# Optimization experiments

Hardware: AMD Instinct MI355X
Metric: run time of the kernel (lower is better)

The kernel has to match this reference:

```python
import jax, jax.numpy as jnp
import numpy as np

B, S, F = 32, 4096, 256
G, N = 2, 128           # num_groups, num_entries_per_group
D = F // G              # group_dim = 128
E = 256                 # embed_dim


def setup_inputs() -> dict:
    key = jax.random.key(0)
    ks = jax.random.split(key, 6)
    return {
        "features": jax.random.normal(ks[0], (B, S, F), jnp.float32),
        "gumbel": jax.random.gumbel(ks[1], (B, S, G, N), jnp.float32),
        "W_logits": jax.random.normal(ks[2], (G, D, N), jnp.float32) * (1.0 / np.sqrt(D)),
        "b_logits": jnp.zeros((G, N), jnp.float32),
        "codebooks": jax.random.normal(ks[3], (G, N, D), jnp.float32) * 0.02,
        "W_out": jax.random.normal(ks[4], (F, E), jnp.float32) * (1.0 / np.sqrt(F)),
        "b_out": jnp.zeros((E,), jnp.float32),
    }


def reference(features, gumbel, W_logits, b_logits, codebooks, W_out, b_out):
    b, s, f = features.shape
    grouped = features.reshape(b, s, G, D)                       # [B,S,G,D]
    logits = jnp.einsum("bsgd,gdn->bsgn", grouped, W_logits) + b_logits
    noisy = logits + gumbel                                      # training=True
    soft = jax.nn.softmax(noisy, axis=-1)                        # [B,S,G,N]
    hard_idx = jnp.argmax(noisy, axis=-1)                        # [B,S,G] int
    hard = jax.nn.one_hot(hard_idx, N, dtype=soft.dtype)
    st = jax.lax.stop_gradient(hard - soft) + soft               # straight-through
    quantized = jnp.einsum("bsgn,gnd->bsgd", st, codebooks)      # [B,S,G,D]
    quantized = quantized.reshape(b, s, G * D)                   # [B,S,F]
    out = quantized @ W_out + b_out                              # [B,S,E]
    indices = hard_idx.astype(jnp.int32)                         # [B,S,G]
    return out, indices
```

## Files before the change

kernel.cpp:

```cpp
#include <hip/hip_runtime.h>

#define T_TOTAL (32 * 4096)
#define FDIM 256
#define NG 2
#define NN 128
#define DDIM 128
#define EDIM 256

#define TAU 0.004f
#define CAP 16384

typedef __attribute__((ext_vector_type(4))) float f32x4;
typedef __attribute__((ext_vector_type(8))) short short8;

__global__ __launch_bounds__(256) void prep_kernel(
    const float* __restrict__ codebooks,
    const float* __restrict__ W_out,
    const float* __restrict__ Wl,
    float* __restrict__ CO,
    short* __restrict__ BT,
    int* __restrict__ flag_count)
{
    const int gn  = blockIdx.x;
    const int g   = gn >> 7;
    const int tid = threadIdx.x;
    __shared__ float cb[DDIM];
    if (tid < DDIM) cb[tid] = codebooks[gn * DDIM + tid];
    if (tid >= 128) {
        const int k = tid - 128;
        const int n = gn & 127;
        const float x = Wl[((size_t)g * DDIM + k) * NN + n];
        const unsigned u = __float_as_uint(x);
        const float hi = __uint_as_float(u & 0xffff0000u);
        const unsigned u2 = __float_as_uint(x - hi);
        BT[(size_t)g * 16384 + n * 128 + k] = (short)(u >> 16);
        BT[32768 + (size_t)g * 16384 + n * 128 + k] = (short)(u2 >> 16);
    }
    if (gn == 0 && tid == 0) *flag_count = 0;
    __syncthreads();
    float acc = 0.f;
    const float* wcol = W_out + (g * DDIM) * EDIM + tid;
#pragma unroll 4
    for (int d = 0; d < DDIM; ++d) acc += cb[d] * wcol[d * EDIM];
    CO[gn * EDIM + tid] = acc;
}

__global__ __launch_bounds__(512) void logits_lds4_kernel(
    const float* __restrict__ features,
    const float* __restrict__ gumbel,
    const short* __restrict__ BT,
    const float* __restrict__ bl,
    float* __restrict__ idx_f,
    int* __restrict__ flag_count,
    int* __restrict__ flag_list)
{
    __shared__ short8 Wlds[4096];

    const int tid = threadIdx.x;
    const int g   = blockIdx.x & 1;
    const int gb  = blockIdx.x >> 1;
    const int w   = tid >> 6;
    const int l   = tid & 63;
    const int q   = l & 15;
    const int h   = l >> 4;

    {
        const short8* src = reinterpret_cast<const short8*>(BT) + g * 2048;
#pragma unroll
        for (int i = 0; i < 8; ++i) {
            const int S   = tid + i * 512;
            const int lev = S >> 11;
            const int n   = (S >> 4) & 127;
            const int sl  = S & 15;
            Wlds[lev * 2048 + n * 16 + (sl ^ (n & 15))] = src[lev * 4096 + n * 16 + sl];
        }
    }
    __syncthreads();

    f32x4 bv[8];
#pragma unroll
    for (int nt = 0; nt < 8; ++nt)
        bv[nt] = *reinterpret_cast<const f32x4*>(bl + g * NN + nt * 16 + h * 4);

    const int t0 = gb * 256 + w * 16 + q;
    const float* fbase = features + (size_t)t0 * FDIM + g * DDIM + h * 8;
    const float* gbase = gumbel + ((size_t)t0 * NG + g) * NN + h * 4;

    f32x4 FA[8], FB[8], GA[8];

#pragma unroll
    for (int j = 0; j < 8; ++j)
        FA[j] = *reinterpret_cast<const f32x4*>(fbase + (j >> 1) * 32 + (j & 1) * 4);

#define PQ_ITER(Fc, Fn, IT)                                                     \
    {                                                                           \
        const float* gp = gbase + (size_t)(IT) * 128 * NG * NN;                 \
        _Pragma("unroll")                                                       \
        for (int nt = 0; nt < 8; ++nt)                                          \
            GA[nt] = *reinterpret_cast<const f32x4*>(gp + nt * 16);             \
        if ((IT) < 1) {                                                         \
            const float* fp = fbase + (size_t)((IT) + 1) * 128 * FDIM;          \
            _Pragma("unroll")                                                   \
            for (int j = 0; j < 8; ++j)                                         \
                Fn[j] = *reinterpret_cast<const f32x4*>(fp + (j >> 1) * 32 + (j & 1) * 4); \
        }                                                                       \
        f32x4 acc[8];                                                           \
        _Pragma("unroll")                                                       \
        for (int nt = 0; nt < 8; ++nt) acc[nt] = (f32x4){0.f, 0.f, 0.f, 0.f};   \
        _Pragma("unroll")                                                       \
        for (int ks = 0; ks < 4; ++ks) {                                        \
            short8 B1, B2;                                                      \
            _Pragma("unroll")                                                   \
            for (int e = 0; e < 4; ++e) {                                       \
                const unsigned ua = __float_as_uint(Fc[2 * ks][e]);             \
                const float ha = __uint_as_float(ua & 0xffff0000u);             \
                const unsigned ra = __float_as_uint(Fc[2 * ks][e] - ha);        \
                B1[e] = (short)(ua >> 16);                                      \
                B2[e] = (short)(ra >> 16);                                      \
                const unsigned ub = __float_as_uint(Fc[2 * ks + 1][e]);         \
                const float hb = __uint_as_float(ub & 0xffff0000u);             \
                const unsigned rb = __float_as_uint(Fc[2 * ks + 1][e] - hb);    \
                B1[4 + e] = (short)(ub >> 16);                                  \
                B2[4 + e] = (short)(rb >> 16);                                  \
            }                                                                   \
            _Pragma("unroll")                                                   \
            for (int nt = 0; nt < 8; ++nt) {                                    \
                const int base = (nt * 16 + q) * 16 + ((ks * 4 + h) ^ q);       \
                const short8 A1 = Wlds[base];                                   \
                const short8 A2 = Wlds[2048 + base];                            \
                acc[nt] = __builtin_amdgcn_mfma_f32_16x16x32_bf16(A1, B1, acc[nt], 0, 0, 0); \
                acc[nt] = __builtin_amdgcn_mfma_f32_16x16x32_bf16(A2, B1, acc[nt], 0, 0, 0); \
                acc[nt] = __builtin_amdgcn_mfma_f32_16x16x32_bf16(A1, B2, acc[nt], 0, 0, 0); \
            }                                                                   \
        }                                                                       \
        float m1 = -3.4e38f, m2 = -3.4e38f;                                     \
        int   i1 = 0;                                                           \
        _Pragma("unroll")                                                       \
        for (int nt = 0; nt < 8; ++nt) {                                        \
            _Pragma("unroll")                                                   \
            for (int r = 0; r < 4; ++r) {                                       \
                const float vv = acc[nt][r] + bv[nt][r] + GA[nt][r];            \
                const int   n  = nt * 16 + h * 4 + r;                           \
                if (vv > m1) { m2 = m1; m1 = vv; i1 = n; }                      \
                else         { m2 = fmaxf(m2, vv); }                            \
            }                                                                   \
        }                                                                       \
        _Pragma("unroll")                                                       \
        for (int off = 16; off < 64; off <<= 1) {                               \
            const float om1 = __shfl_xor(m1, off);                              \
            const int   oi1 = __shfl_xor(i1, off);                              \
            const float om2 = __shfl_xor(m2, off);                              \
            if (om1 > m1)      { m2 = fmaxf(m1, om2); m1 = om1; i1 = oi1; }     \
            else if (om1 < m1) { m2 = fmaxf(m2, om1); }                         \
            else               { m2 = m1; i1 = min(i1, oi1); }                  \
        }                                                                       \
        if (h == 0) {                                                           \
            const int t = t0 + (IT) * 128;                                      \
            idx_f[(size_t)t * NG + g] = (float)i1;                              \
            if (m1 - m2 < TAU) {                                                \
                const int p = atomicAdd(flag_count, 1);                         \
                if (p < CAP) flag_list[p] = t * NG + g;                         \
            }                                                                   \
        }                                                                       \
    }

    PQ_ITER(FA, FB, 0)
    PQ_ITER(FB, FA, 1)
#undef PQ_ITER
}

__global__ __launch_bounds__(128) void fixup_kernel(
    const float* __restrict__ features,
    const float* __restrict__ gumbel,
    const float* __restrict__ Wl,
    const float* __restrict__ bl,
    float* __restrict__ idx_f,
    const int* __restrict__ flag_count,
    const int* __restrict__ flag_list)
{
    __shared__ float sm[2];
    __shared__ int   si[2];
    int total = *flag_count;
    if (total > CAP) total = CAP;
    const int n = threadIdx.x;

    for (int e = blockIdx.x; e < total; e += gridDim.x) {
        const int code = flag_list[e];
        const int t = code >> 1, g = code & 1;
        const float* fpr = features + (size_t)t * FDIM + g * DDIM;
        const float* wp  = Wl + (size_t)g * DDIM * NN + n;
        float dot = 0.f;
#pragma unroll 8
        for (int k = 0; k < DDIM; ++k) dot = fmaf(fpr[k], wp[(size_t)k * NN], dot);
        const float v = (dot + bl[g * NN + n]) + gumbel[((size_t)t * NG + g) * NN + n];

        float m = v; int bi = n;
#pragma unroll
        for (int off = 1; off < 64; off <<= 1) {
            const float om = __shfl_xor(m, off);
            const int   ob = __shfl_xor(bi, off);
            if (om > m || (om == m && ob < bi)) { m = om; bi = ob; }
        }
        if ((n & 63) == 0) { sm[n >> 6] = m; si[n >> 6] = bi; }
        __syncthreads();
        if (n == 0) {
            const float mA = sm[0], mB = sm[1];
            const int bA = si[0], bB = si[1];
            const int best = (mB > mA || (mB == mA && bB < bA)) ? bB : bA;
            idx_f[code] = (float)best;
        }
        __syncthreads();
    }
}

__global__ __launch_bounds__(256) void out_kernel(
    const float* __restrict__ CO,
    const float* __restrict__ b_out,
    const float* __restrict__ idx_f,
    float* __restrict__ out)
{
    const int tid = threadIdx.x;
    const int e4  = tid & 63;
    const int ts  = tid >> 6;
    const int tbase = blockIdx.x * 16;
    const float4 b = *reinterpret_cast<const float4*>(b_out + e4 * 4);

#pragma unroll
    for (int it = 0; it < 4; ++it) {
        const int t  = tbase + it * 4 + ts;
        const int i0 = (int)idx_f[t * NG + 0];
        const int i1 = (int)idx_f[t * NG + 1];
        const float4 c0 = *reinterpret_cast<const float4*>(CO + (size_t)i0 * EDIM + e4 * 4);
        const float4 c1 = *reinterpret_cast<const float4*>(CO + (size_t)(NN + i1) * EDIM + e4 * 4);
        float4 o;
        o.x = c0.x + c1.x + b.x;
        o.y = c0.y + c1.y + b.y;
        o.z = c0.z + c1.z + b.z;
        o.w = c0.w + c1.w + b.w;
        *reinterpret_cast<float4*>(out + (size_t)t * EDIM + e4 * 4) = o;
    }
}

extern "C" void kernel_launch(void* const* d_in, const int* in_sizes, int n_in,
                              void* d_out, int out_size, void* d_ws, size_t ws_size,
                              hipStream_t stream) {
    const float* features  = (const float*)d_in[0];
    const float* gumbel    = (const float*)d_in[1];
    const float* Wl        = (const float*)d_in[2];
    const float* bl        = (const float*)d_in[3];
    const float* codebooks = (const float*)d_in[4];
    const float* W_out     = (const float*)d_in[5];
    const float* b_out     = (const float*)d_in[6];

    float* out   = (float*)d_out;
    float* idx_f = out + (size_t)T_TOTAL * EDIM;

    char* ws = (char*)d_ws;
    float* CO         = (float*)ws;
    short* BT         = (short*)(ws + 262144);
    int*   flag_count = (int*)(ws + 262144 + 131072);
    int*   flag_list  = (int*)(ws + 393216 + 256);

    prep_kernel<<<NG * NN, 256, 0, stream>>>(codebooks, W_out, Wl, CO, BT, flag_count);
    logits_lds4_kernel<<<1024, 512, 0, stream>>>(
        features, gumbel, BT, bl, idx_f, flag_count, flag_list);
    fixup_kernel<<<1024, 128, 0, stream>>>(
        features, gumbel, Wl, bl, idx_f, flag_count, flag_list);
    out_kernel<<<T_TOTAL / 16, 256, 0, stream>>>(CO, b_out, idx_f, out);
}
```

Before: 124.5 us.

## Process four token tiles per block with inline-asm loads and explicit waits

Halves the grid and has each block handle four 128-token iterations instead of two, which spreads the LDS weight staging over more work. Feature and gumbel loads are issued through inline-asm global_load_dwordx4 with manual s_waitcnt barriers, so the gumbel load overlaps the MFMA loop and the next feature tile is fetched before the argmax. The bias now comes from shared memory instead of being held in registers, freeing VGPRs. The trade-offs are fewer blocks to fill the GPU, and manual waits that fully drain vmcnt, which may serialise loads the compiler could otherwise overlap.

After: 118.7 us, median of 2. -4.6%, faster.

```diff
diff --git a/kernel.cpp b/kernel.cpp
--- a/kernel.cpp
+++ b/kernel.cpp
@@ -45,7 +45,7 @@
     CO[gn * EDIM + tid] = acc;
 }
 
-__global__ __launch_bounds__(512) void logits_lds4_kernel(
+__global__ __launch_bounds__(512) void pq_v16_kernel(
     const float* __restrict__ features,
     const float* __restrict__ gumbel,
     const short* __restrict__ BT,
@@ -55,6 +55,7 @@
     int* __restrict__ flag_list)
 {
     __shared__ short8 Wlds[4096];
+    __shared__ float  bl_s[NN];
 
     const int tid = threadIdx.x;
     const int g   = blockIdx.x & 1;
@@ -74,35 +75,35 @@
             const int sl  = S & 15;
             Wlds[lev * 2048 + n * 16 + (sl ^ (n & 15))] = src[lev * 4096 + n * 16 + sl];
         }
+        if (tid < NN) bl_s[tid] = bl[g * NN + tid];
     }
     __syncthreads();
 
-    f32x4 bv[8];
-#pragma unroll
-    for (int nt = 0; nt < 8; ++nt)
-        bv[nt] = *reinterpret_cast<const f32x4*>(bl + g * NN + nt * 16 + h * 4);
-
-    const int t0 = gb * 256 + w * 16 + q;
+    const int t0 = gb * 512 + w * 16 + q;
     const float* fbase = features + (size_t)t0 * FDIM + g * DDIM + h * 8;
     const float* gbase = gumbel + ((size_t)t0 * NG + g) * NN + h * 4;
 
-    f32x4 FA[8], FB[8], GA[8];
+    f32x4 F[8], GA[8];
+
+#define GLOAD(dst, ptr) \
+    asm volatile("global_load_dwordx4 %0, %1, off" : "=v"(dst) : "v"(ptr))
+#define VWAIT() do { \
+    asm volatile("s_waitcnt vmcnt(0)" ::: "memory"); \
+    __builtin_amdgcn_sched_barrier(0); } while (0)
 
 #pragma unroll
     for (int j = 0; j < 8; ++j)
-        FA[j] = *reinterpret_cast<const f32x4*>(fbase + (j >> 1) * 32 + (j & 1) * 4);
-
-#define PQ_ITER(Fc, Fn, IT)                                                     \
+        GLOAD(F[j], fbase + (j >> 1) * 32 + (j & 1) * 4);
+
+#define PQ_IT(IT)                                                               \
     {                                                                           \
-        const float* gp = gbase + (size_t)(IT) * 128 * NG * NN;                 \
-        _Pragma("unroll")                                                       \
-        for (int nt = 0; nt < 8; ++nt)                                          \
-            GA[nt] = *reinterpret_cast<const f32x4*>(gp + nt * 16);             \
-        if ((IT) < 1) {                                                         \
-            const float* fp = fbase + (size_t)((IT) + 1) * 128 * FDIM;          \
-            _Pragma("unroll")                                                   \
-            for (int j = 0; j < 8; ++j)                                         \
-                Fn[j] = *reinterpret_cast<const f32x4*>(fp + (j >> 1) * 32 + (j & 1) * 4); \
+        VWAIT();         \
+                               \
+        {                                                                       \
+            const float* gp = gbase + (size_t)(IT) * 128 * NG * NN;             \
+            _Pragma("unroll")                                                   \
+            for (int nt = 0; nt < 8; ++nt)                                      \
+                GLOAD(GA[nt], gp + nt * 16);                                    \
         }                                                                       \
         f32x4 acc[8];                                                           \
         _Pragma("unroll")                                                       \
@@ -112,14 +113,14 @@
             short8 B1, B2;                                                      \
             _Pragma("unroll")                                                   \
             for (int e = 0; e < 4; ++e) {                                       \
-                const unsigned ua = __float_as_uint(Fc[2 * ks][e]);             \
+                const unsigned ua = __float_as_uint(F[2 * ks][e]);              \
                 const float ha = __uint_as_float(ua & 0xffff0000u);             \
-                const unsigned ra = __float_as_uint(Fc[2 * ks][e] - ha);        \
+                const unsigned ra = __float_as_uint(F[2 * ks][e] - ha);         \
                 B1[e] = (short)(ua >> 16);                                      \
                 B2[e] = (short)(ra >> 16);                                      \
-                const unsigned ub = __float_as_uint(Fc[2 * ks + 1][e]);         \
+                const unsigned ub = __float_as_uint(F[2 * ks + 1][e]);          \
                 const float hb = __uint_as_float(ub & 0xffff0000u);             \
-                const unsigned rb = __float_as_uint(Fc[2 * ks + 1][e] - hb);    \
+                const unsigned rb = __float_as_uint(F[2 * ks + 1][e] - hb);     \
                 B1[4 + e] = (short)(ub >> 16);                                  \
                 B2[4 + e] = (short)(rb >> 16);                                  \
             }                                                                   \
@@ -133,13 +134,23 @@
                 acc[nt] = __builtin_amdgcn_mfma_f32_16x16x32_bf16(A1, B2, acc[nt], 0, 0, 0); \
             }                                                                   \
         }                                                                       \
+        VWAIT();       \
+                        \
+        if ((IT) < 3) {                                                         \
+            const float* fp = fbase + (size_t)((IT) + 1) * 128 * FDIM;          \
+            _Pragma("unroll")                                                   \
+            for (int j = 0; j < 8; ++j)                                         \
+                GLOAD(F[j], fp + (j >> 1) * 32 + (j & 1) * 4);                  \
+        }                                                                       \
+                          \
         float m1 = -3.4e38f, m2 = -3.4e38f;                                     \
         int   i1 = 0;                                                           \
         _Pragma("unroll")                                                       \
         for (int nt = 0; nt < 8; ++nt) {                                        \
+            const f32x4 bvr = *reinterpret_cast<const f32x4*>(&bl_s[nt * 16 + h * 4]); \
             _Pragma("unroll")                                                   \
             for (int r = 0; r < 4; ++r) {                                       \
-                const float vv = acc[nt][r] + bv[nt][r] + GA[nt][r];            \
+                const float vv = acc[nt][r] + bvr[r] + GA[nt][r];               \
                 const int   n  = nt * 16 + h * 4 + r;                           \
                 if (vv > m1) { m2 = m1; m1 = vv; i1 = n; }                      \
                 else         { m2 = fmaxf(m2, vv); }                            \
@@ -164,9 +175,13 @@
         }                                                                       \
     }
 
-    PQ_ITER(FA, FB, 0)
-    PQ_ITER(FB, FA, 1)
-#undef PQ_ITER
+    PQ_IT(0)
+    PQ_IT(1)
+    PQ_IT(2)
+    PQ_IT(3)
+#undef PQ_IT
+#undef GLOAD
+#undef VWAIT
 }
 
 __global__ __launch_bounds__(128) void fixup_kernel(
@@ -262,7 +277,7 @@
     int*   flag_list  = (int*)(ws + 393216 + 256);
 
     prep_kernel<<<NG * NN, 256, 0, stream>>>(codebooks, W_out, Wl, CO, BT, flag_count);
-    logits_lds4_kernel<<<1024, 512, 0, stream>>>(
+    pq_v16_kernel<<<512, 512, 0, stream>>>(
         features, gumbel, BT, bl, idx_f, flag_count, flag_list);
     fixup_kernel<<<1024, 128, 0, stream>>>(
         features, gumbel, Wl, bl, idx_f, flag_count, flag_list);
```
